# Kernel optimization log

Measured on AMD Instinct MI355X. Metric: run time of the kernel, lower is better.

## Reference

```python
import jax, jax.numpy as jnp
import numpy as np

N_NODES = 100000
N_EDGES = 3200000
N_GRAPHS = 256
IN_CH = 8
HID = 64
N_REL = 2


def rgcn_conv(x, edge_index, edge_type, W, root, bias):
    # W: [R, in, out]; PyG RGCNConv with aggr='mean' per relation, summed across relations
    n = x.shape[0]
    src, dst = edge_index[0], edge_index[1]
    H = jnp.einsum('ni,rio->rno', x, W)                      # [R, N, out]
    msgs = H[edge_type, src]                                  # [E, out]
    # per-(node, relation) in-degree for the mean
    seg = dst * N_REL + edge_type
    deg = jax.ops.segment_sum(jnp.ones_like(edge_type, dtype=x.dtype), seg,
                              num_segments=n * N_REL)
    norm = jnp.maximum(deg[seg], 1.0)
    agg = jax.ops.segment_sum(msgs / norm[:, None], dst, num_segments=n)  # [N, out]
    return agg + x @ root + bias


def setup_inputs() -> dict:
    key = jax.random.key(0)
    ks = jax.random.split(key, 16)
    x = jax.random.normal(ks[0], (N_NODES, IN_CH), dtype=jnp.float32)
    edge_index = jax.random.randint(ks[1], (2, N_EDGES), 0, N_NODES, dtype=jnp.int64)
    edge_type = jax.random.randint(ks[2], (N_EDGES,), 0, N_REL, dtype=jnp.int64)
    batch = jnp.sort(jax.random.randint(ks[3], (N_NODES,), 0, N_GRAPHS, dtype=jnp.int64))

    def glorot(k, shape):
        fan_in, fan_out = shape[-2], shape[-1]
        s = float(np.sqrt(6.0 / (fan_in + fan_out)))
        return jax.random.uniform(k, shape, dtype=jnp.float32, minval=-s, maxval=s)

    params = {
        'W1': glorot(ks[4], (N_REL, IN_CH, HID)), 'root1': glorot(ks[5], (IN_CH, HID)),
        'b1': jnp.zeros((HID,), jnp.float32),
        'W2': glorot(ks[6], (N_REL, HID, HID)), 'root2': glorot(ks[7], (HID, HID)),
        'b2': jnp.zeros((HID,), jnp.float32),
        'W3': glorot(ks[8], (N_REL, HID, HID)), 'root3': glorot(ks[9], (HID, HID)),
        'b3': jnp.zeros((HID,), jnp.float32),
        'cW1': glorot(ks[10], (HID, HID // 2)), 'cb1': jnp.zeros((HID // 2,), jnp.float32),
        'cW2': glorot(ks[11], (HID // 2, 1)), 'cb2': jnp.zeros((1,), jnp.float32),
    }
    return {'x': x, 'edge_index': edge_index, 'edge_type': edge_type, 'batch': batch, **params}


def reference(x, edge_index, edge_type, batch,
              W1, root1, b1, W2, root2, b2, W3, root3, b3,
              cW1, cb1, cW2, cb2):
    h = jax.nn.relu(rgcn_conv(x, edge_index, edge_type, W1, root1, b1))
    h = jax.nn.relu(rgcn_conv(h, edge_index, edge_type, W2, root2, b2))
    h = rgcn_conv(h, edge_index, edge_type, W3, root3, b3)
    g = jax.ops.segment_sum(h, batch, num_segments=N_GRAPHS)   # global_add_pool
    # dropout is identity in eval mode
    g = jax.nn.relu(g @ cW1 + cb1)
    return g @ cW2 + cb2                                        # [N_GRAPHS, 1]
```

## Files before the change

kernel.cpp:

```cpp
#include <hip/hip_runtime.h>


typedef unsigned int uint;
typedef unsigned short ushort;
typedef __attribute__((ext_vector_type(8))) short bf16x8;
typedef __attribute__((ext_vector_type(4))) float f32x4;
typedef __attribute__((ext_vector_type(2))) float f32x2;

#define EPB 6144
#define BCAP 8960

__device__ __forceinline__ uint bf1(float f){
  uint u = __float_as_uint(f);
  return (u + 0x7fffu + ((u>>16)&1u)) >> 16;
}
__device__ __forceinline__ uint bfpack2(float lo, float hi){
  return bf1(lo) | (bf1(hi)<<16);
}
__device__ __forceinline__ f32x2 cvt2lo(uint w){
  f32x2 r; r.x = __uint_as_float(w<<16); r.y = __uint_as_float(w & 0xffff0000u);
  return r;
}
__device__ __forceinline__ void red2(f32x2& a){
  a.x += __shfl_xor(a.x,16); a.x += __shfl_xor(a.x,32);
  a.y += __shfl_xor(a.y,16); a.y += __shfl_xor(a.y,32);
}
__device__ __forceinline__ void acc2(uint2 w, float sg,
    f32x2& tL, f32x2& tH, f32x2& dL, f32x2& dH){
  f32x2 lo = cvt2lo(w.x), hi = cvt2lo(w.y);
  f32x2 s2 = {sg, sg};
  tL += lo; tH += hi;
  dL += s2*lo; dH += s2*hi;
}

__global__ __launch_bounds__(1024) void k_part(const int* __restrict__ ei,
    const int* __restrict__ et, int* __restrict__ bcur,
    uint* __restrict__ bk, int E, int NBK){
  __shared__ int h[400];
  __shared__ int cur[400];
  int t = threadIdx.x;
  for (int i=t;i<NBK;i+=1024) h[i]=0;
  __syncthreads();
  int base = blockIdx.x*EPB;
  for (int i=t; i<EPB; i+=1024){
    int e = base+i;
    if (e < E) atomicAdd(&h[ei[E+e]>>8], 1);
  }
  __syncthreads();
  for (int i=t;i<NBK;i+=1024){
    int c = h[i];
    cur[i] = c ? (i*BCAP + atomicAdd(&bcur[i], c)) : 0;
  }
  __syncthreads();
  int e0=base+t,      e1=base+t+1024, e2=base+t+2048;
  int e3=base+t+3072, e4=base+t+4096, e5=base+t+5120;
  bool v0=e0<E, v1=e1<E, v2=e2<E, v3=e3<E, v4=e4<E, v5=e5<E;
  int s0=0,d0=0,y0=0,s1=0,d1=0,y1=0,s2=0,d2=0,y2=0;
  int s3=0,d3=0,y3=0,s4=0,d4=0,y4=0,s5=0,d5=0,y5=0;
  if (v0){ s0=ei[e0]; d0=ei[E+e0]; y0=et[e0]; }
  if (v1){ s1=ei[e1]; d1=ei[E+e1]; y1=et[e1]; }
  if (v2){ s2=ei[e2]; d2=ei[E+e2]; y2=et[e2]; }
  if (v3){ s3=ei[e3]; d3=ei[E+e3]; y3=et[e3]; }
  if (v4){ s4=ei[e4]; d4=ei[E+e4]; y4=et[e4]; }
  if (v5){ s5=ei[e5]; d5=ei[E+e5]; y5=et[e5]; }
  if (v0){
    int bu=d0>>8, p=atomicAdd(&cur[bu],1);
    if (p < (bu+1)*BCAP) bk[p] = ((uint)s0<<9)|(uint)(((d0&255)<<1)|y0);
  }
  if (v1){
    int bu=d1>>8, p=atomicAdd(&cur[bu],1);
    if (p < (bu+1)*BCAP) bk[p] = ((uint)s1<<9)|(uint)(((d1&255)<<1)|y1);
  }
  if (v2){
    int bu=d2>>8, p=atomicAdd(&cur[bu],1);
    if (p < (bu+1)*BCAP) bk[p] = ((uint)s2<<9)|(uint)(((d2&255)<<1)|y2);
  }
  if (v3){
    int bu=d3>>8, p=atomicAdd(&cur[bu],1);
    if (p < (bu+1)*BCAP) bk[p] = ((uint)s3<<9)|(uint)(((d3&255)<<1)|y3);
  }
  if (v4){
    int bu=d4>>8, p=atomicAdd(&cur[bu],1);
    if (p < (bu+1)*BCAP) bk[p] = ((uint)s4<<9)|(uint)(((d4&255)<<1)|y4);
  }
  if (v5){
    int bu=d5>>8, p=atomicAdd(&cur[bu],1);
    if (p < (bu+1)*BCAP) bk[p] = ((uint)s5<<9)|(uint)(((d5&255)<<1)|y5);
  }
}

__global__ __launch_bounds__(1024) void k_csr(const uint* __restrict__ bk,
    const int* __restrict__ bcur, int* __restrict__ deg,
    int* __restrict__ pos, int* __restrict__ ssrc, int N,
    const float* __restrict__ W2, const float* __restrict__ root2,
    const float* __restrict__ W3, const float* __restrict__ root3,
    ushort* __restrict__ wt2, ushort* __restrict__ wt3,
    float* __restrict__ gp, ushort* __restrict__ h1z,
    ushort* __restrict__ h2z, int NBK, int G){
  int b = blockIdx.x, t = threadIdx.x;
  if (b >= NBK){
    const float* Wl = (b==NBK) ? W2 : W3;
    const float* rp = (b==NBK) ? root2 : root3;
    ushort* wt = (b==NBK) ? wt2 : wt3;
    for (int i=t; i<64*192; i+=1024){
      int n = i/192, k = i - n*192;
      float v = (k<128) ? Wl[k*64+n] : rp[(k-128)*64+n];
      wt[i] = (ushort)bf1(v);
    }
    if (b==NBK+1){
      for (int i=t;i<G*64;i+=1024) gp[i]=0.f;
      if (t < 64){
        h1z[(size_t)N*64 + t] = 0;
        h2z[(size_t)N*64 + t] = 0;
      }
    }
    return;
  }
  __shared__ int h[512];
  __shared__ int cur[512];
  __shared__ int ws[256];
  int start = b*BCAP;
  int cnt = bcur[b]; if (cnt > BCAP) cnt = BCAP;
  int end = start + cnt;
  if (t < 512) h[t]=0;
  __syncthreads();
  for (int i=start+t; i<end; i+=1024) atomicAdd(&h[bk[i]&511], 1);
  __syncthreads();
  int c0=0, c1=0, s=0;
  if (t < 256){
    c0=h[2*t]; c1=h[2*t+1]; s=c0+c1;
    ws[t] = s;
  }
  __syncthreads();
  for (int off=1; off<256; off<<=1){
    int tmp = (t>=off && t<256)? ws[t-off]:0;
    __syncthreads();
    if (t<256) ws[t] += tmp;
    __syncthreads();
  }
  if (t < 256){
    int base0 = start + ws[t] - s;
    cur[2*t]   = base0;
    cur[2*t+1] = base0 + c0;
    int node = (b<<8) + t;
    if (node < N){
      deg[(b<<9)+2*t]   = c0; deg[(b<<9)+2*t+1] = c1;
      pos[(b<<9)+2*t]   = base0; pos[(b<<9)+2*t+1] = base0 + c0;
    }
  }
  __syncthreads();
  for (int i=start+t; i<end; i+=1024){
    uint w = bk[i];
    int p = atomicAdd(&cur[w & 511], 1);
    ssrc[p] = (int)(w >> 9);
  }
}

__global__ __launch_bounds__(256) void k_gather64(
    const ushort* __restrict__ hp, const int* __restrict__ deg,
    const int* __restrict__ pos, const int* __restrict__ ssrc,
    ushort* __restrict__ sn, int N)
{
  int lane = threadIdx.x & 63;
  int wid  = (blockIdx.x*256 + threadIdx.x) >> 6;
  int c4 = lane & 15, eg = lane >> 4;
  int nA = wid*2, nB = nA+1;
  if (nA >= N) return;
  int d0A = __builtin_amdgcn_readfirstlane(deg[2*nA]);
  int d1A = __builtin_amdgcn_readfirstlane(deg[2*nA+1]);
  int pA  = __builtin_amdgcn_readfirstlane(pos[2*nA]);
  int cA  = d0A + d1A;
  int d0B = 0, d1B = 0, pB = 0, cB = 0;
  if (nB < N){
    d0B = __builtin_amdgcn_readfirstlane(deg[2*nB]);
    d1B = __builtin_amdgcn_readfirstlane(deg[2*nB+1]);
    pB  = __builtin_amdgcn_readfirstlane(pos[2*nB]);
    cB  = d0B+d1B;
  }

  f32x2 totAL={0,0}, totAH={0,0}, difAL={0,0}, difAH={0,0};
  f32x2 totBL={0,0}, totBH={0,0}, difBL={0,0}, difBH={0,0};
  int jA = 0, jB = 0;
  while (jA < cA || jB < cB){
    int tA = cA - jA; if (tA > 64) tA = 64;
    int tB = cB - jB; if (tB > 64) tB = 64;
    int r0A = d0A - jA, r0B = d0B - jB;
    int svA = N, svB = N;
    if (lane < tA) svA = ssrc[pA + jA + lane];
    if (lane < tB) svB = ssrc[pB + jB + lane];
    float ssA = (lane < r0A) ? 1.f : -1.f;
    float ssB = (lane < r0B) ? 1.f : -1.f;
    int mt = tA > tB ? tA : tB;
    for (int e = 0; e < mt; e += 8){
      int i0 = e + eg, i1 = e + 4 + eg;
      int a0 = __shfl(svA, i0), b0 = __shfl(svB, i0);
      int a1 = __shfl(svA, i1), b1 = __shfl(svB, i1);
      float sA0 = __shfl(ssA, i0), sB0 = __shfl(ssB, i0);
      float sA1 = __shfl(ssA, i1), sB1 = __shfl(ssB, i1);
      uint2 wA0 = *(const uint2*)(hp + (size_t)a0*64 + c4*4);
      uint2 wB0 = *(const uint2*)(hp + (size_t)b0*64 + c4*4);
      uint2 wA1 = *(const uint2*)(hp + (size_t)a1*64 + c4*4);
      uint2 wB1 = *(const uint2*)(hp + (size_t)b1*64 + c4*4);
      acc2(wA0, sA0, totAL, totAH, difAL, difAH);
      acc2(wB0, sB0, totBL, totBH, difBL, difBH);
      acc2(wA1, sA1, totAL, totAH, difAL, difAH);
      acc2(wB1, sB1, totBL, totBH, difBL, difBH);
    }
    jA += tA; jB += tB;
  }
  red2(totAL); red2(totAH); red2(difAL); red2(difAH);
  red2(totBL); red2(totBH); red2(difBL); red2(difBH);
  int rel = (lane >> 4) & 1;
  float4 tt_, dd_;
  if (lane < 32){
    tt_ = make_float4(totAL.x, totAL.y, totAH.x, totAH.y);
    dd_ = make_float4(difAL.x, difAL.y, difAH.x, difAH.y);
  } else {
    tt_ = make_float4(totBL.x, totBL.y, totBH.x, totBH.y);
    dd_ = make_float4(difBL.x, difBL.y, difBH.x, difBH.y);
  }
  int dsel = (lane < 32) ? (rel ? d1A : d0A) : (rel ? d1B : d0B);
  float sg = rel ? -1.f : 1.f;
  float id = 0.5f / (float)(dsel > 1 ? dsel : 1);
  float4 v;
  v.x = fmaf(sg, dd_.x, tt_.x) * id;
  v.y = fmaf(sg, dd_.y, tt_.y) * id;
  v.z = fmaf(sg, dd_.z, tt_.z) * id;
  v.w = fmaf(sg, dd_.w, tt_.w) * id;
  int n = (lane < 32) ? nA : nB;
  if (n < N){
    uint2 pkt; pkt.x = bfpack2(v.x, v.y); pkt.y = bfpack2(v.z, v.w);
    *(uint2*)(sn + (size_t)n*128 + rel*64 + c4*4) = pkt;
  }
}

__global__ __launch_bounds__(256) void k_l1(
    const float* __restrict__ xp, const int* __restrict__ deg,
    const int* __restrict__ pos, const int* __restrict__ ssrc,
    const float* __restrict__ W1,
    const float* __restrict__ root1,
    const float* __restrict__ b1,
    ushort* __restrict__ h1, int N)
{
  int lane = threadIdx.x & 63;
  int wid  = (blockIdx.x*256 + threadIdx.x) >> 6;
  int c = lane & 7, eg = lane >> 3;
  int nA = wid*2, nB = nA+1;
  if (nA >= N) return;
  int d0A = deg[2*nA], d1A = deg[2*nA+1];
  int pA  = pos[2*nA];
  int cA  = d0A + d1A;
  int d0B = 0, d1B = 0, pB = 0, cB = 0;
  if (nB < N){ d0B = deg[2*nB]; d1B = deg[2*nB+1]; pB = pos[2*nB]; cB = d0B+d1B; }

  float totA=0.f, s1A=0.f, totB=0.f, s1B=0.f;
  int jA = 0, jB = 0;
  while (jA < cA || jB < cB){
    int tA = cA - jA; if (tA > 64) tA = 64;
    int tB = cB - jB; if (tB > 64) tB = 64;
    int svA = (lane < tA) ? ssrc[pA + jA + lane] : 0;
    int svB = (lane < tB) ? ssrc[pB + jB + lane] : 0;
    int mt = tA > tB ? tA : tB;
    for (int e = 0; e < mt; e += 16){
      int i0 = e + eg, i1 = e + 8 + eg;
      int a0 = __shfl(svA, i0), a1 = __shfl(svA, i1);
      int b0 = __shfl(svB, i0), b1 = __shfl(svB, i1);
      float vA0 = xp[(size_t)a0*8 + c];
      float vA1 = xp[(size_t)a1*8 + c];
      float vB0 = xp[(size_t)b0*8 + c];
      float vB1 = xp[(size_t)b1*8 + c];
      vA0 = (i0 < tA) ? vA0 : 0.f;
      vA1 = (i1 < tA) ? vA1 : 0.f;
      vB0 = (i0 < tB) ? vB0 : 0.f;
      vB1 = (i1 < tB) ? vB1 : 0.f;
      totA += vA0;  s1A += ((jA + i0) >= d0A) ? vA0 : 0.f;
      totA += vA1;  s1A += ((jA + i1) >= d0A) ? vA1 : 0.f;
      totB += vB0;  s1B += ((jB + i0) >= d0B) ? vB0 : 0.f;
      totB += vB1;  s1B += ((jB + i1) >= d0B) ? vB1 : 0.f;
    }
    jA += tA; jB += tB;
  }
  float s0A = totA - s1A, s0B = totB - s1B;
  #pragma unroll
  for (int off=8; off<64; off<<=1){
    s0A += __shfl_xor(s0A, off); s1A += __shfl_xor(s1A, off);
    s0B += __shfl_xor(s0B, off); s1B += __shfl_xor(s1B, off);
  }
  s0A *= 1.f/(float)(d0A>1?d0A:1);  s1A *= 1.f/(float)(d1A>1?d1A:1);
  s0B *= 1.f/(float)(d0B>1?d0B:1);  s1B *= 1.f/(float)(d1B>1?d1B:1);

  int ch = lane;
  float accA = b1[ch], accB = accA;
  #pragma unroll
  for (int k = 0; k < 8; ++k){
    float wv = W1[k*64 + ch];
    accA = fmaf(__shfl(s0A, k), wv, accA);
    accB = fmaf(__shfl(s0B, k), wv, accB);
  }
  #pragma unroll
  for (int k = 0; k < 8; ++k){
    float wv = W1[512 + k*64 + ch];
    accA = fmaf(__shfl(s1A, k), wv, accA);
    accB = fmaf(__shfl(s1B, k), wv, accB);
  }
  #pragma unroll
  for (int k = 0; k < 8; ++k){
    float wr = root1[k*64 + ch];
    float xa = xp[(size_t)nA*8 + k];
    accA = fmaf(xa, wr, accA);
    if (nB < N){
      float xb = xp[(size_t)nB*8 + k];
      accB = fmaf(xb, wr, accB);
    }
  }
  accA = fmaxf(accA, 0.f);
  h1[(size_t)nA*64 + ch] = (ushort)bf1(accA);
  if (nB < N){
    accB = fmaxf(accB, 0.f);
    h1[(size_t)nB*64 + ch] = (ushort)bf1(accB);
  }
}

template<int RELU, int OUTBF>
__global__ __launch_bounds__(256) void k_mm192m(
    const ushort* __restrict__ sn,
    const ushort* __restrict__ hp,
    const ushort* __restrict__ wt,
    const float* __restrict__ bias, void* __restrict__ hout_, int N)
{
  int t = threadIdx.x, lane = t & 63, w = t >> 6;
  int quad = lane >> 4, l15 = lane & 15;
  int nb = blockIdx.x * 64;
  int node = nb + w*16 + l15;
  int ncl = node < N ? node : N-1;
  const ushort* arow_sn = sn + (size_t)ncl*128 + quad*8;
  const ushort* arow_hp = hp + (size_t)ncl*64  + quad*8;

  f32x4 acc0={0,0,0,0}, acc1={0,0,0,0}, acc2_={0,0,0,0}, acc3={0,0,0,0};
  #pragma unroll
  for (int ks = 0; ks < 6; ++ks){
    bf16x8 a = (ks < 4) ? *(const bf16x8*)(arow_sn + ks*32)
                        : *(const bf16x8*)(arow_hp + (ks-4)*32);
    const ushort* wk = wt + (size_t)l15*192 + ks*32 + quad*8;
    bf16x8 b0 = *(const bf16x8*)(wk);
    bf16x8 b1 = *(const bf16x8*)(wk + 16*192);
    bf16x8 b2 = *(const bf16x8*)(wk + 32*192);
    bf16x8 b3 = *(const bf16x8*)(wk + 48*192);
    acc0 = __builtin_amdgcn_mfma_f32_16x16x32_bf16(a, b0, acc0, 0,0,0);
    acc1 = __builtin_amdgcn_mfma_f32_16x16x32_bf16(a, b1, acc1, 0,0,0);
    acc2_ = __builtin_amdgcn_mfma_f32_16x16x32_bf16(a, b2, acc2_, 0,0,0);
    acc3 = __builtin_amdgcn_mfma_f32_16x16x32_bf16(a, b3, acc3, 0,0,0);
  }
  f32x4 accs[4] = {acc0, acc1, acc2_, acc3};
  #pragma unroll
  for (int tt = 0; tt < 4; ++tt){
    int n = tt*16 + l15;
    float bv = bias[n];
    #pragma unroll
    for (int i = 0; i < 4; ++i){
      int nd = nb + w*16 + quad*4 + i;
      if (nd < N){
        float v = accs[tt][i] + bv;
        if (RELU) v = fmaxf(v, 0.f);
        if (OUTBF) ((ushort*)hout_)[(size_t)nd*64 + n] = (ushort)bf1(v);
        else       ((float*)hout_)[(size_t)nd*64 + n] = v;
      }
    }
  }
}

__global__ __launch_bounds__(256) void k_mm192pool(
    const ushort* __restrict__ sn, const ushort* __restrict__ hp,
    const ushort* __restrict__ wt, const float* __restrict__ bias,
    const int* __restrict__ batch, float* __restrict__ gp, int N)
{
  __shared__ float hl[64*66];
  __shared__ int bl[64];
  int t = threadIdx.x, lane = t & 63, w = t >> 6;
  int quad = lane >> 4, l15 = lane & 15;
  int nb = blockIdx.x * 64;
  int node = nb + w*16 + l15;
  int ncl = node < N ? node : N-1;
  const ushort* arow_sn = sn + (size_t)ncl*128 + quad*8;
  const ushort* arow_hp = hp + (size_t)ncl*64  + quad*8;

  f32x4 acc0={0,0,0,0}, acc1={0,0,0,0}, acc2_={0,0,0,0}, acc3={0,0,0,0};
  #pragma unroll
  for (int ks = 0; ks < 6; ++ks){
    bf16x8 a = (ks < 4) ? *(const bf16x8*)(arow_sn + ks*32)
                        : *(const bf16x8*)(arow_hp + (ks-4)*32);
    const ushort* wk = wt + (size_t)l15*192 + ks*32 + quad*8;
    bf16x8 b0 = *(const bf16x8*)(wk);
    bf16x8 b1 = *(const bf16x8*)(wk + 16*192);
    bf16x8 b2 = *(const bf16x8*)(wk + 32*192);
    bf16x8 b3 = *(const bf16x8*)(wk + 48*192);
    acc0 = __builtin_amdgcn_mfma_f32_16x16x32_bf16(a, b0, acc0, 0,0,0);
    acc1 = __builtin_amdgcn_mfma_f32_16x16x32_bf16(a, b1, acc1, 0,0,0);
    acc2_ = __builtin_amdgcn_mfma_f32_16x16x32_bf16(a, b2, acc2_, 0,0,0);
    acc3 = __builtin_amdgcn_mfma_f32_16x16x32_bf16(a, b3, acc3, 0,0,0);
  }
  f32x4 accs[4] = {acc0, acc1, acc2_, acc3};
  #pragma unroll
  for (int tt = 0; tt < 4; ++tt){
    int ch = tt*16 + l15;
    float bv = bias[ch];
    #pragma unroll
    for (int i = 0; i < 4; ++i){
      int nl = w*16 + quad*4 + i;
      hl[nl*66 + ch] = accs[tt][i] + bv;
    }
  }
  if (t < 64) bl[t] = (nb + t < N) ? batch[nb + t] : -1;
  __syncthreads();
  int c = t & 63, q = t >> 6;
  float acc = 0.f; int curg = -1;
  #pragma unroll 4
  for (int i = 0; i < 16; ++i){
    int nl = q*16 + i;
    int g = bl[nl];
    if (g != curg){
      if (curg >= 0) atomicAdd(&gp[curg*64 + c], acc);
      curg = g; acc = 0.f;
    }
    if (g >= 0) acc += hl[nl*66 + c];
  }
  if (curg >= 0) atomicAdd(&gp[curg*64 + c], acc);
}

__global__ __launch_bounds__(256) void k_clf(const float* __restrict__ gp,
    const float* __restrict__ cW1, const float* __restrict__ cb1,
    const float* __restrict__ cW2, const float* __restrict__ cb2,
    float* __restrict__ out, int G){
  int lane = threadIdx.x & 63;
  int g = (blockIdx.x*256 + threadIdx.x) >> 6;
  if (g >= G) return;
  int j = lane & 31, half = lane >> 5;
  const float* gv = gp + (size_t)g*64 + half*32;
  const float* Wc = cW1 + half*32*32 + j;
  float s = 0.f;
  #pragma unroll 8
  for (int i=0;i<32;++i) s += gv[i] * Wc[i*32];
  s += __shfl_xor(s, 32);
  s = fmaxf(s + cb1[j], 0.f) * cW2[j];
  s += __shfl_xor(s, 1);  s += __shfl_xor(s, 2);
  s += __shfl_xor(s, 4);  s += __shfl_xor(s, 8);
  s += __shfl_xor(s, 16);
  if (lane == 0) out[g] = s + cb2[0];
}

extern "C" void kernel_launch(void* const* d_in, const int* in_sizes, int n_in,
                              void* d_out, int out_size, void* d_ws, size_t ws_size,
                              hipStream_t stream){
  const float* x     = (const float*)d_in[0];
  const int*   ei    = (const int*)d_in[1];
  const int*   et    = (const int*)d_in[2];
  const int*   batch = (const int*)d_in[3];
  const float* W1    = (const float*)d_in[4];
  const float* root1 = (const float*)d_in[5];
  const float* b1    = (const float*)d_in[6];
  const float* W2    = (const float*)d_in[7];
  const float* root2 = (const float*)d_in[8];
  const float* b2    = (const float*)d_in[9];
  const float* W3    = (const float*)d_in[10];
  const float* root3 = (const float*)d_in[11];
  const float* b3    = (const float*)d_in[12];
  const float* cW1   = (const float*)d_in[13];
  const float* cb1   = (const float*)d_in[14];
  const float* cW2   = (const float*)d_in[15];
  const float* cb2   = (const float*)d_in[16];
  float* out = (float*)d_out;
  (void)n_in; (void)ws_size;

  int N = in_sizes[0]/8;
  int E = in_sizes[2];
  int G = out_size;
  int M = 2*N;
  int NBK = (N + 255) >> 8;

  char* w = (char*)d_ws;
  auto alloc=[&](size_t bytes)->char*{ char* p=w; w += (bytes+255)&~(size_t)255; return p; };
  int*    bcur  = (int*)alloc(1024*4);
  int*    ssrc  = (int*)alloc((size_t)NBK*BCAP*4);
  int*    deg   = (int*)alloc((size_t)M*4);
  int*    pos   = (int*)alloc((size_t)M*4);
  ushort* h1    = (ushort*)alloc((size_t)(N+1)*64*2);
  ushort* snU   = (ushort*)alloc((size_t)N*128*2);
  ushort* h2    = (ushort*)alloc((size_t)(N+1)*64*2);
  float*  gp    = (float*)alloc((size_t)G*64*4);
  ushort* wt2   = (ushort*)alloc(64*192*2);
  ushort* wt3   = (ushort*)alloc(64*192*2);
  uint*   bk    = (uint*)snU;

  hipMemsetAsync(bcur, 0, (size_t)NBK*4, stream);
  int nbE = (E + EPB - 1)/EPB;
  k_part <<<nbE,1024,0,stream>>>(ei,et,bcur,bk,E,NBK);
  k_csr  <<<NBK+2,1024,0,stream>>>(bk,bcur,deg,pos,ssrc,N,
                                   W2,root2,W3,root3,wt2,wt3,gp,h1,h2,NBK,G);

  int gb = (((N+1)/2) + 3) / 4;
  int nbk = (N+63)/64;
  k_l1<<<gb,256,0,stream>>>(x,deg,pos,ssrc,W1,root1,b1,h1,N);
  k_gather64<<<gb,256,0,stream>>>(h1,deg,pos,ssrc,snU,N);
  k_mm192m<1,1><<<nbk,256,0,stream>>>(snU,h1,wt2,b2,h2,N);
  k_gather64<<<gb,256,0,stream>>>(h2,deg,pos,ssrc,snU,N);
  k_mm192pool<<<nbk,256,0,stream>>>(snU,h2,wt3,b3,batch,gp,N);
  k_clf<<<(G*64+255)/256,256,0,stream>>>(gp,cW1,cb1,cW2,cb2,out,G);
}
```

Baseline: 361.4 us.

## Fuse neighbor gather into MFMA layer kernel via shared-memory staging

```diff
diff --git a/kernel.cpp b/kernel.cpp
--- a/kernel.cpp
+++ b/kernel.cpp
@@ -9,6 +9,7 @@
 
 #define EPB 6144
 #define BCAP 8960
+#define ASTR 136
 
 __device__ __forceinline__ uint bf1(float f){
   uint u = __float_as_uint(f);
@@ -153,84 +154,6 @@
     uint w = bk[i];
     int p = atomicAdd(&cur[w & 511], 1);
     ssrc[p] = (int)(w >> 9);
-  }
-}
-
-__global__ __launch_bounds__(256) void k_gather64(
-    const ushort* __restrict__ hp, const int* __restrict__ deg,
-    const int* __restrict__ pos, const int* __restrict__ ssrc,
-    ushort* __restrict__ sn, int N)
-{
-  int lane = threadIdx.x & 63;
-  int wid  = (blockIdx.x*256 + threadIdx.x) >> 6;
-  int c4 = lane & 15, eg = lane >> 4;
-  int nA = wid*2, nB = nA+1;
-  if (nA >= N) return;
-  int d0A = __builtin_amdgcn_readfirstlane(deg[2*nA]);
-  int d1A = __builtin_amdgcn_readfirstlane(deg[2*nA+1]);
-  int pA  = __builtin_amdgcn_readfirstlane(pos[2*nA]);
-  int cA  = d0A + d1A;
-  int d0B = 0, d1B = 0, pB = 0, cB = 0;
-  if (nB < N){
-    d0B = __builtin_amdgcn_readfirstlane(deg[2*nB]);
-    d1B = __builtin_amdgcn_readfirstlane(deg[2*nB+1]);
-    pB  = __builtin_amdgcn_readfirstlane(pos[2*nB]);
-    cB  = d0B+d1B;
-  }
-
-  f32x2 totAL={0,0}, totAH={0,0}, difAL={0,0}, difAH={0,0};
-  f32x2 totBL={0,0}, totBH={0,0}, difBL={0,0}, difBH={0,0};
-  int jA = 0, jB = 0;
-  while (jA < cA || jB < cB){
-    int tA = cA - jA; if (tA > 64) tA = 64;
-    int tB = cB - jB; if (tB > 64) tB = 64;
-    int r0A = d0A - jA, r0B = d0B - jB;
-    int svA = N, svB = N;
-    if (lane < tA) svA = ssrc[pA + jA + lane];
-    if (lane < tB) svB = ssrc[pB + jB + lane];
-    float ssA = (lane < r0A) ? 1.f : -1.f;
-    float ssB = (lane < r0B) ? 1.f : -1.f;
-    int mt = tA > tB ? tA : tB;
-    for (int e = 0; e < mt; e += 8){
-      int i0 = e + eg, i1 = e + 4 + eg;
-      int a0 = __shfl(svA, i0), b0 = __shfl(svB, i0);
-      int a1 = __shfl(svA, i1), b1 = __shfl(svB, i1);
-      float sA0 = __shfl(ssA, i0), sB0 = __shfl(ssB, i0);
-      float sA1 = __shfl(ssA, i1), sB1 = __shfl(ssB, i1);
-      uint2 wA0 = *(const uint2*)(hp + (size_t)a0*64 + c4*4);
-      uint2 wB0 = *(const uint2*)(hp + (size_t)b0*64 + c4*4);
-      uint2 wA1 = *(const uint2*)(hp + (size_t)a1*64 + c4*4);
-      uint2 wB1 = *(const uint2*)(hp + (size_t)b1*64 + c4*4);
-      acc2(wA0, sA0, totAL, totAH, difAL, difAH);
-      acc2(wB0, sB0, totBL, totBH, difBL, difBH);
-      acc2(wA1, sA1, totAL, totAH, difAL, difAH);
-      acc2(wB1, sB1, totBL, totBH, difBL, difBH);
-    }
-    jA += tA; jB += tB;
-  }
-  red2(totAL); red2(totAH); red2(difAL); red2(difAH);
-  red2(totBL); red2(totBH); red2(difBL); red2(difBH);
-  int rel = (lane >> 4) & 1;
-  float4 tt_, dd_;
-  if (lane < 32){
-    tt_ = make_float4(totAL.x, totAL.y, totAH.x, totAH.y);
-    dd_ = make_float4(difAL.x, difAL.y, difAH.x, difAH.y);
-  } else {
-    tt_ = make_float4(totBL.x, totBL.y, totBH.x, totBH.y);
-    dd_ = make_float4(difBL.x, difBL.y, difBH.x, difBH.y);
-  }
-  int dsel = (lane < 32) ? (rel ? d1A : d0A) : (rel ? d1B : d0B);
-  float sg = rel ? -1.f : 1.f;
-  float id = 0.5f / (float)(dsel > 1 ? dsel : 1);
-  float4 v;
-  v.x = fmaf(sg, dd_.x, tt_.x) * id;
-  v.y = fmaf(sg, dd_.y, tt_.y) * id;
-  v.z = fmaf(sg, dd_.z, tt_.z) * id;
-  v.w = fmaf(sg, dd_.w, tt_.w) * id;
-  int n = (lane < 32) ? nA : nB;
-  if (n < N){
-    uint2 pkt; pkt.x = bfpack2(v.x, v.y); pkt.y = bfpack2(v.z, v.w);
-    *(uint2*)(sn + (size_t)n*128 + rel*64 + c4*4) = pkt;
   }
 }
 
@@ -321,25 +244,100 @@
   }
 }
 
-template<int RELU, int OUTBF>
-__global__ __launch_bounds__(256) void k_mm192m(
-    const ushort* __restrict__ sn,
+template<int POOL>
+__global__ __launch_bounds__(256) void k_gmm(
     const ushort* __restrict__ hp,
+    const int* __restrict__ deg, const int* __restrict__ pos,
+    const int* __restrict__ ssrc,
     const ushort* __restrict__ wt,
-    const float* __restrict__ bias, void* __restrict__ hout_, int N)
+    const float* __restrict__ bias,
+    const int* __restrict__ batch,
+    void* __restrict__ outp,
+    int N)
 {
+  __shared__ __align__(16) ushort Asm[64*ASTR];
+  __shared__ int bl[64];
   int t = threadIdx.x, lane = t & 63, w = t >> 6;
+  int c4 = lane & 15, eg = lane >> 4;
+  int nb = blockIdx.x * 64;
+
+  for (int r = 0; r < 8; ++r){
+    int nA = nb + w*16 + r*2, nB = nA + 1;
+    int iA = nA < N ? nA : 0, iB = nB < N ? nB : 0;
+    int d0A = __builtin_amdgcn_readfirstlane(deg[2*iA]);
+    int d1A = __builtin_amdgcn_readfirstlane(deg[2*iA+1]);
+    int pA  = __builtin_amdgcn_readfirstlane(pos[2*iA]);
+    int d0B = __builtin_amdgcn_readfirstlane(deg[2*iB]);
+    int d1B = __builtin_amdgcn_readfirstlane(deg[2*iB+1]);
+    int pB  = __builtin_amdgcn_readfirstlane(pos[2*iB]);
+    if (nA >= N){ d0A = 0; d1A = 0; }
+    if (nB >= N){ d0B = 0; d1B = 0; }
+    int cA = d0A + d1A, cB = d0B + d1B;
+
+    f32x2 totAL={0,0}, totAH={0,0}, difAL={0,0}, difAH={0,0};
+    f32x2 totBL={0,0}, totBH={0,0}, difBL={0,0}, difBH={0,0};
+    int jA = 0, jB = 0;
+    while (jA < cA || jB < cB){
+      int tA = cA - jA; if (tA > 64) tA = 64;
+      int tB = cB - jB; if (tB > 64) tB = 64;
+      int r0A = d0A - jA, r0B = d0B - jB;
+      int svA = N, svB = N;
+      if (lane < tA) svA = ssrc[pA + jA + lane];
+      if (lane < tB) svB = ssrc[pB + jB + lane];
+      float ssA = (lane < r0A) ? 1.f : -1.f;
+      float ssB = (lane < r0B) ? 1.f : -1.f;
+      int mt = tA > tB ? tA : tB;
+      for (int e = 0; e < mt; e += 8){
+        int i0 = e + eg, i1 = e + 4 + eg;
+        int a0 = __shfl(svA, i0), b0 = __shfl(svB, i0);
+        int a1 = __shfl(svA, i1), b1 = __shfl(svB, i1);
+        float sA0 = __shfl(ssA, i0), sB0 = __shfl(ssB, i0);
+        float sA1 = __shfl(ssA, i1), sB1 = __shfl(ssB, i1);
+        uint2 wA0 = *(const uint2*)(hp + (size_t)a0*64 + c4*4);
+        uint2 wB0 = *(const uint2*)(hp + (size_t)b0*64 + c4*4);
+        uint2 wA1 = *(const uint2*)(hp + (size_t)a1*64 + c4*4);
+        uint2 wB1 = *(const uint2*)(hp + (size_t)b1*64 + c4*4);
+        acc2(wA0, sA0, totAL, totAH, difAL, difAH);
+        acc2(wB0, sB0, totBL, totBH, difBL, difBH);
+        acc2(wA1, sA1, totAL, totAH, difAL, difAH);
+        acc2(wB1, sB1, totBL, totBH, difBL, difBH);
+      }
+      jA += tA; jB += tB;
+    }
+    red2(totAL); red2(totAH); red2(difAL); red2(difAH);
+    red2(totBL); red2(totBH); red2(difBL); red2(difBH);
+    int rel = (lane >> 4) & 1;
+    float4 tt_, dd_;
+    if (lane < 32){
+      tt_ = make_float4(totAL.x, totAL.y, totAH.x, totAH.y);
+      dd_ = make_float4(difAL.x, difAL.y, difAH.x, difAH.y);
+    } else {
+      tt_ = make_float4(totBL.x, totBL.y, totBH.x, totBH.y);
+      dd_ = make_float4(difBL.x, difBL.y, difBH.x, difBH.y);
+    }
+    int dsel = (lane < 32) ? (rel ? d1A : d0A) : (rel ? d1B : d0B);
+    float sg = rel ? -1.f : 1.f;
+    float id = 0.5f / (float)(dsel > 1 ? dsel : 1);
+    float4 v;
+    v.x = fmaf(sg, dd_.x, tt_.x) * id;
+    v.y = fmaf(sg, dd_.y, tt_.y) * id;
+    v.z = fmaf(sg, dd_.z, tt_.z) * id;
+    v.w = fmaf(sg, dd_.w, tt_.w) * id;
+    int nl = ((lane < 32) ? nA : nB) - nb;
+    uint2 pkt; pkt.x = bfpack2(v.x, v.y); pkt.y = bfpack2(v.z, v.w);
+    *(uint2*)(Asm + nl*ASTR + rel*64 + c4*4) = pkt;
+  }
+
   int quad = lane >> 4, l15 = lane & 15;
-  int nb = blockIdx.x * 64;
   int node = nb + w*16 + l15;
   int ncl = node < N ? node : N-1;
-  const ushort* arow_sn = sn + (size_t)ncl*128 + quad*8;
-  const ushort* arow_hp = hp + (size_t)ncl*64  + quad*8;
+  const ushort* arow_hp = hp + (size_t)ncl*64 + quad*8;
+  const ushort* arow_sm = Asm + (w*16 + l15)*ASTR + quad*8;
 
   f32x4 acc0={0,0,0,0}, acc1={0,0,0,0}, acc2_={0,0,0,0}, acc3={0,0,0,0};
   #pragma unroll
   for (int ks = 0; ks < 6; ++ks){
-    bf16x8 a = (ks < 4) ? *(const bf16x8*)(arow_sn + ks*32)
+    bf16x8 a = (ks < 4) ? *(const bf16x8*)(arow_sm + ks*32)
                         : *(const bf16x8*)(arow_hp + (ks-4)*32);
     const ushort* wk = wt + (size_t)l15*192 + ks*32 + quad*8;
     bf16x8 b0 = *(const bf16x8*)(wk);
@@ -352,79 +350,52 @@
     acc3 = __builtin_amdgcn_mfma_f32_16x16x32_bf16(a, b3, acc3, 0,0,0);
   }
   f32x4 accs[4] = {acc0, acc1, acc2_, acc3};
-  #pragma unroll
-  for (int tt = 0; tt < 4; ++tt){
-    int n = tt*16 + l15;
-    float bv = bias[n];
+
+  if (!POOL){
+    ushort* hout = (ushort*)outp;
     #pragma unroll
-    for (int i = 0; i < 4; ++i){
-      int nd = nb + w*16 + quad*4 + i;
-      if (nd < N){
-        float v = accs[tt][i] + bv;
-        if (RELU) v = fmaxf(v, 0.f);
-        if (OUTBF) ((ushort*)hout_)[(size_t)nd*64 + n] = (ushort)bf1(v);
-        else       ((float*)hout_)[(size_t)nd*64 + n] = v;
+    for (int tt = 0; tt < 4; ++tt){
+      int n = tt*16 + l15;
+      float bv = bias[n];
+      #pragma unroll
+      for (int i = 0; i < 4; ++i){
+        int nd = nb + w*16 + quad*4 + i;
+        if (nd < N){
+          float v = fmaxf(accs[tt][i] + bv, 0.f);
+          hout[(size_t)nd*64 + n] = (ushort)bf1(v);
+        }
       }
     }
-  }
-}
-
-__global__ __launch_bounds__(256) void k_mm192pool(
-    const ushort* __restrict__ sn, const ushort* __restrict__ hp,
-    const ushort* __restrict__ wt, const float* __restrict__ bias,
-    const int* __restrict__ batch, float* __restrict__ gp, int N)
-{
-  __shared__ float hl[64*66];
-  __shared__ int bl[64];
-  int t = threadIdx.x, lane = t & 63, w = t >> 6;
-  int quad = lane >> 4, l15 = lane & 15;
-  int nb = blockIdx.x * 64;
-  int node = nb + w*16 + l15;
-  int ncl = node < N ? node : N-1;
-  const ushort* arow_sn = sn + (size_t)ncl*128 + quad*8;
-  const ushort* arow_hp = hp + (size_t)ncl*64  + quad*8;
-
-  f32x4 acc0={0,0,0,0}, acc1={0,0,0,0}, acc2_={0,0,0,0}, acc3={0,0,0,0};
-  #pragma unroll
-  for (int ks = 0; ks < 6; ++ks){
-    bf16x8 a = (ks < 4) ? *(const bf16x8*)(arow_sn + ks*32)
-                        : *(const bf16x8*)(arow_hp + (ks-4)*32);
-    const ushort* wk = wt + (size_t)l15*192 + ks*32 + quad*8;
-    bf16x8 b0 = *(const bf16x8*)(wk);
-    bf16x8 b1 = *(const bf16x8*)(wk + 16*192);
-    bf16x8 b2 = *(const bf16x8*)(wk + 32*192);
-    bf16x8 b3 = *(const bf16x8*)(wk + 48*192);
-    acc0 = __builtin_amdgcn_mfma_f32_16x16x32_bf16(a, b0, acc0, 0,0,0);
-    acc1 = __builtin_amdgcn_mfma_f32_16x16x32_bf16(a, b1, acc1, 0,0,0);
-    acc2_ = __builtin_amdgcn_mfma_f32_16x16x32_bf16(a, b2, acc2_, 0,0,0);
-    acc3 = __builtin_amdgcn_mfma_f32_16x16x32_bf16(a, b3, acc3, 0,0,0);
-  }
-  f32x4 accs[4] = {acc0, acc1, acc2_, acc3};
-  #pragma unroll
-  for (int tt = 0; tt < 4; ++tt){
-    int ch = tt*16 + l15;
-    float bv = bias[ch];
+  } else {
+    float* gp = (float*)outp;
+    __syncthreads();
+    float* hl = (float*)Asm;
     #pragma unroll
-    for (int i = 0; i < 4; ++i){
-      int nl = w*16 + quad*4 + i;
-      hl[nl*66 + ch] = accs[tt][i] + bv;
-    }
-  }
-  if (t < 64) bl[t] = (nb + t < N) ? batch[nb + t] : -1;
-  __syncthreads();
-  int c = t & 63, q = t >> 6;
-  float acc = 0.f; int curg = -1;
-  #pragma unroll 4
-  for (int i = 0; i < 16; ++i){
-    int nl = q*16 + i;
-    int g = bl[nl];
-    if (g != curg){
-      if (curg >= 0) atomicAdd(&gp[curg*64 + c], acc);
-      curg = g; acc = 0.f;
-    }
-    if (g >= 0) acc += hl[nl*66 + c];
-  }
-  if (curg >= 0) atomicAdd(&gp[curg*64 + c], acc);
+    for (int tt = 0; tt < 4; ++tt){
+      int ch = tt*16 + l15;
+      float bv = bias[ch];
+      #pragma unroll
+      for (int i = 0; i < 4; ++i){
+        int nl = w*16 + quad*4 + i;
+        hl[nl*66 + ch] = accs[tt][i] + bv;
+      }
+    }
+    if (t < 64) bl[t] = (nb + t < N) ? batch[nb + t] : -1;
+    __syncthreads();
+    int c = t & 63, q = t >> 6;
+    float acc = 0.f; int curg = -1;
+    #pragma unroll 4
+    for (int i = 0; i < 16; ++i){
+      int nl = q*16 + i;
+      int g = bl[nl];
+      if (g != curg){
+        if (curg >= 0) atomicAdd(&gp[curg*64 + c], acc);
+        curg = g; acc = 0.f;
+      }
+      if (g >= 0) acc += hl[nl*66 + c];
+    }
+    if (curg >= 0) atomicAdd(&gp[curg*64 + c], acc);
+  }
 }
 
 __global__ __launch_bounds__(256) void k_clf(const float* __restrict__ gp,
@@ -481,15 +452,14 @@
   auto alloc=[&](size_t bytes)->char*{ char* p=w; w += (bytes+255)&~(size_t)255; return p; };
   int*    bcur  = (int*)alloc(1024*4);
   int*    ssrc  = (int*)alloc((size_t)NBK*BCAP*4);
+  uint*   bk    = (uint*)alloc((size_t)NBK*BCAP*4);
   int*    deg   = (int*)alloc((size_t)M*4);
   int*    pos   = (int*)alloc((size_t)M*4);
   ushort* h1    = (ushort*)alloc((size_t)(N+1)*64*2);
-  ushort* snU   = (ushort*)alloc((size_t)N*128*2);
   ushort* h2    = (ushort*)alloc((size_t)(N+1)*64*2);
   float*  gp    = (float*)alloc((size_t)G*64*4);
   ushort* wt2   = (ushort*)alloc(64*192*2);
   ushort* wt3   = (ushort*)alloc(64*192*2);
-  uint*   bk    = (uint*)snU;
 
   hipMemsetAsync(bcur, 0, (size_t)NBK*4, stream);
   int nbE = (E + EPB - 1)/EPB;
@@ -500,9 +470,7 @@
   int gb = (((N+1)/2) + 3) / 4;
   int nbk = (N+63)/64;
   k_l1<<<gb,256,0,stream>>>(x,deg,pos,ssrc,W1,root1,b1,h1,N);
-  k_gather64<<<gb,256,0,stream>>>(h1,deg,pos,ssrc,snU,N);
-  k_mm192m<1,1><<<nbk,256,0,stream>>>(snU,h1,wt2,b2,h2,N);
-  k_gather64<<<gb,256,0,stream>>>(h2,deg,pos,ssrc,snU,N);
-  k_mm192pool<<<nbk,256,0,stream>>>(snU,h2,wt3,b3,batch,gp,N);
+  k_gmm<0><<<nbk,256,0,stream>>>(h1,deg,pos,ssrc,wt2,b2,batch,h2,N);
+  k_gmm<1><<<nbk,256,0,stream>>>(h2,deg,pos,ssrc,wt3,b3,batch,gp,N);
   k_clf<<<(G*64+255)/256,256,0,stream>>>(gp,cW1,cb1,cW2,cb2,out,G);
 }
```

After: 373.4 us. +3.3%, slower.

## Stage partitioned edges in LDS for coalesced bucket writes and single bk read

Applied to the files above, without the earlier changes.

```diff
diff --git a/kernel.cpp b/kernel.cpp
--- a/kernel.cpp
+++ b/kernel.cpp
@@ -36,22 +36,16 @@
 __global__ __launch_bounds__(1024) void k_part(const int* __restrict__ ei,
     const int* __restrict__ et, int* __restrict__ bcur,
     uint* __restrict__ bk, int E, int NBK){
+  __shared__ uint   stg[EPB];
+  __shared__ ushort stgb[EPB];
   __shared__ int h[400];
-  __shared__ int cur[400];
+  __shared__ int basep[400];
+  __shared__ int loc[400];
+  __shared__ int sc[512];
+  __shared__ int tot_s;
   int t = threadIdx.x;
-  for (int i=t;i<NBK;i+=1024) h[i]=0;
-  __syncthreads();
   int base = blockIdx.x*EPB;
-  for (int i=t; i<EPB; i+=1024){
-    int e = base+i;
-    if (e < E) atomicAdd(&h[ei[E+e]>>8], 1);
-  }
-  __syncthreads();
-  for (int i=t;i<NBK;i+=1024){
-    int c = h[i];
-    cur[i] = c ? (i*BCAP + atomicAdd(&bcur[i], c)) : 0;
-  }
-  __syncthreads();
+
   int e0=base+t,      e1=base+t+1024, e2=base+t+2048;
   int e3=base+t+3072, e4=base+t+4096, e5=base+t+5120;
   bool v0=e0<E, v1=e1<E, v2=e2<E, v3=e3<E, v4=e4<E, v5=e5<E;
@@ -63,29 +57,45 @@
   if (v3){ s3=ei[e3]; d3=ei[E+e3]; y3=et[e3]; }
   if (v4){ s4=ei[e4]; d4=ei[E+e4]; y4=et[e4]; }
   if (v5){ s5=ei[e5]; d5=ei[E+e5]; y5=et[e5]; }
-  if (v0){
-    int bu=d0>>8, p=atomicAdd(&cur[bu],1);
-    if (p < (bu+1)*BCAP) bk[p] = ((uint)s0<<9)|(uint)(((d0&255)<<1)|y0);
-  }
-  if (v1){
-    int bu=d1>>8, p=atomicAdd(&cur[bu],1);
-    if (p < (bu+1)*BCAP) bk[p] = ((uint)s1<<9)|(uint)(((d1&255)<<1)|y1);
-  }
-  if (v2){
-    int bu=d2>>8, p=atomicAdd(&cur[bu],1);
-    if (p < (bu+1)*BCAP) bk[p] = ((uint)s2<<9)|(uint)(((d2&255)<<1)|y2);
-  }
-  if (v3){
-    int bu=d3>>8, p=atomicAdd(&cur[bu],1);
-    if (p < (bu+1)*BCAP) bk[p] = ((uint)s3<<9)|(uint)(((d3&255)<<1)|y3);
-  }
-  if (v4){
-    int bu=d4>>8, p=atomicAdd(&cur[bu],1);
-    if (p < (bu+1)*BCAP) bk[p] = ((uint)s4<<9)|(uint)(((d4&255)<<1)|y4);
-  }
-  if (v5){
-    int bu=d5>>8, p=atomicAdd(&cur[bu],1);
-    if (p < (bu+1)*BCAP) bk[p] = ((uint)s5<<9)|(uint)(((d5&255)<<1)|y5);
+
+  for (int i=t;i<NBK;i+=1024) h[i]=0;
+  __syncthreads();
+  int r0=0,r1=0,r2=0,r3=0,r4=0,r5=0;
+  if (v0) r0 = atomicAdd(&h[d0>>8], 1);
+  if (v1) r1 = atomicAdd(&h[d1>>8], 1);
+  if (v2) r2 = atomicAdd(&h[d2>>8], 1);
+  if (v3) r3 = atomicAdd(&h[d3>>8], 1);
+  if (v4) r4 = atomicAdd(&h[d4>>8], 1);
+  if (v5) r5 = atomicAdd(&h[d5>>8], 1);
+  __syncthreads();
+  if (t < 512) sc[t] = (t < NBK) ? h[t] : 0;
+  __syncthreads();
+  for (int off=1; off<512; off<<=1){
+    int v=0;
+    if (t<512 && t>=off) v = sc[t-off];
+    __syncthreads();
+    if (t<512) sc[t] += v;
+    __syncthreads();
+  }
+  if (t < NBK){
+    int c = h[t];
+    basep[t] = c ? (t*BCAP + atomicAdd(&bcur[t], c)) : 0;
+    loc[t]   = sc[t] - c;
+  }
+  if (t == 511) tot_s = sc[511];
+  __syncthreads();
+  if (v0){ int bu=d0>>8, p=loc[bu]+r0; stg[p]=((uint)s0<<9)|(uint)(((d0&255)<<1)|y0); stgb[p]=(ushort)bu; }
+  if (v1){ int bu=d1>>8, p=loc[bu]+r1; stg[p]=((uint)s1<<9)|(uint)(((d1&255)<<1)|y1); stgb[p]=(ushort)bu; }
+  if (v2){ int bu=d2>>8, p=loc[bu]+r2; stg[p]=((uint)s2<<9)|(uint)(((d2&255)<<1)|y2); stgb[p]=(ushort)bu; }
+  if (v3){ int bu=d3>>8, p=loc[bu]+r3; stg[p]=((uint)s3<<9)|(uint)(((d3&255)<<1)|y3); stgb[p]=(ushort)bu; }
+  if (v4){ int bu=d4>>8, p=loc[bu]+r4; stg[p]=((uint)s4<<9)|(uint)(((d4&255)<<1)|y4); stgb[p]=(ushort)bu; }
+  if (v5){ int bu=d5>>8, p=loc[bu]+r5; stg[p]=((uint)s5<<9)|(uint)(((d5&255)<<1)|y5); stgb[p]=(ushort)bu; }
+  __syncthreads();
+  int tot = tot_s;
+  for (int i=t; i<tot; i+=1024){
+    int bu  = stgb[i];
+    int abs_ = basep[bu] + (i - loc[bu]);
+    if (abs_ < (bu+1)*BCAP) bk[abs_] = stg[i];
   }
 }
 
@@ -97,6 +107,10 @@
     ushort* __restrict__ wt2, ushort* __restrict__ wt3,
     float* __restrict__ gp, ushort* __restrict__ h1z,
     ushort* __restrict__ h2z, int NBK, int G){
+  __shared__ uint stg[BCAP];
+  __shared__ int h[512];
+  __shared__ int cur[512];
+  __shared__ int ws[256];
   int b = blockIdx.x, t = threadIdx.x;
   if (b >= NBK){
     const float* Wl = (b==NBK) ? W2 : W3;
@@ -116,15 +130,12 @@
     }
     return;
   }
-  __shared__ int h[512];
-  __shared__ int cur[512];
-  __shared__ int ws[256];
   int start = b*BCAP;
   int cnt = bcur[b]; if (cnt > BCAP) cnt = BCAP;
-  int end = start + cnt;
   if (t < 512) h[t]=0;
-  __syncthreads();
-  for (int i=start+t; i<end; i+=1024) atomicAdd(&h[bk[i]&511], 1);
+  for (int i=t; i<cnt; i+=1024) stg[i] = bk[start+i];
+  __syncthreads();
+  for (int i=t; i<cnt; i+=1024) atomicAdd(&h[stg[i]&511], 1);
   __syncthreads();
   int c0=0, c1=0, s=0;
   if (t < 256){
@@ -149,8 +160,8 @@
     }
   }
   __syncthreads();
-  for (int i=start+t; i<end; i+=1024){
-    uint w = bk[i];
+  for (int i=t; i<cnt; i+=1024){
+    uint w = stg[i];
     int p = atomicAdd(&cur[w & 511], 1);
     ssrc[p] = (int)(w >> 9);
   }
```

New measurement: 353.6 us. -2.2%, faster.
